# Kernel tuning notes

Hardware: AMD Instinct MI355X
Metric: run time of the kernel (lower is better)

Reference implementation:

```python
import jax, jax.numpy as jnp
import numpy as np

D_MODEL = 1024
PATCH = 16
HID = 256
VOCAB = 256

def setup_inputs() -> dict:
    key = jax.random.key(0)
    ks = jax.random.split(key, 12)
    B, N = 16, 512
    s = lambda *sh: 1.0 / np.sqrt(sh[-1])
    inp = {
        'latents': jax.random.normal(ks[0], (B, N, D_MODEL), dtype=jnp.float32),
        'target_bytes': jax.random.randint(ks[1], (B, N * PATCH), 0, VOCAB, dtype=jnp.int64),
        'W_proj': jax.random.normal(ks[2], (HID, D_MODEL), dtype=jnp.float32) * s(HID, D_MODEL),
        'b_proj': jnp.zeros((HID,), dtype=jnp.float32),
        'emb_table': jax.random.normal(ks[3], (VOCAB, HID), dtype=jnp.float32),
        'W_ih': jax.random.normal(ks[4], (3 * HID, 2 * HID), dtype=jnp.float32) * s(1, 2 * HID),
        'W_hh': jax.random.normal(ks[5], (3 * HID, HID), dtype=jnp.float32) * s(1, HID),
        'b_ih': jnp.zeros((3 * HID,), dtype=jnp.float32),
        'b_hh': jnp.zeros((3 * HID,), dtype=jnp.float32),
        'W_head': jax.random.normal(ks[6], (VOCAB, HID), dtype=jnp.float32) * s(VOCAB, HID),
        'b_head': jnp.zeros((VOCAB,), dtype=jnp.float32),
    }
    return inp

def _gru_scan(x_proj, W_hh, b_hh, h0):
    # x_proj: [T, BN, 3H] precomputed input projections (incl. b_ih)
    def step(h, xg):
        hg = h @ W_hh.T + b_hh                      # [BN, 3H]
        xr, xz, xn = jnp.split(xg, 3, axis=-1)
        hr, hz, hn = jnp.split(hg, 3, axis=-1)
        r = jax.nn.sigmoid(xr + hr)
        z = jax.nn.sigmoid(xz + hz)
        n = jnp.tanh(xn + r * hn)
        h_new = (1.0 - z) * n + z * h
        return h_new, h_new
    _, outs = jax.lax.scan(step, h0, x_proj)
    return outs                                      # [T, BN, H]

def reference(latents, target_bytes, W_proj, b_proj, emb_table, W_ih, W_hh, b_ih, b_hh, W_head, b_head):
    B, N, D = latents.shape
    BN = B * N
    latent_ctx = (latents.reshape(BN, D) @ W_proj.T + b_proj)        # [BN, H]
    targets = target_bytes.reshape(BN, PATCH)
    sos = jnp.zeros((BN, 1), dtype=targets.dtype)
    rnn_in_bytes = jnp.concatenate([sos, targets[:, :-1]], axis=1)   # [BN, P]
    emb = emb_table[rnn_in_bytes]                                    # [BN, P, H]
    lat_exp = jnp.broadcast_to(latent_ctx[:, None, :], (BN, PATCH, HID))
    rnn_input = jnp.concatenate([emb, lat_exp], axis=-1)             # [BN, P, 2H]
    x_proj = jnp.einsum('bpi,gi->bpg', rnn_input, W_ih) + b_ih       # [BN, P, 3H]
    h0 = jnp.zeros((BN, HID), dtype=latents.dtype)
    outs = _gru_scan(jnp.swapaxes(x_proj, 0, 1), W_hh, b_hh, h0)     # [P, BN, H]
    outs = jnp.swapaxes(outs, 0, 1)                                  # [BN, P, H]
    logits = jnp.einsum('bph,vh->bpv', outs, W_head) + b_head        # [BN, P, 256]
    return logits.reshape(B, N, PATCH, VOCAB)
```

## Files before the change

### kernel.cpp

```cpp
#include <hip/hip_runtime.h>
#include <math.h>

#define NSEQ 8192
#define PATCHL 16
#define HIDN 256
#define VOCABN 256

typedef __attribute__((ext_vector_type(4))) float f32x4;
typedef __attribute__((ext_vector_type(8))) short bf16x8;

__device__ __forceinline__ unsigned short f2bf(float f) {
    unsigned int x = __float_as_uint(f);
    unsigned int r = (x + 0x7fffu + ((x >> 16) & 1u)) >> 16;
    return (unsigned short)r;
}
__device__ __forceinline__ float bf2f(unsigned short b) {
    return __uint_as_float(((unsigned int)b) << 16);
}
__device__ __forceinline__ float sigf(float x)   { return 1.f / (1.f + __expf(-x)); }
__device__ __forceinline__ float tanhf_(float x) { return 2.f / (1.f + __expf(-2.f * x)) - 1.f; }

__global__ __launch_bounds__(256)
void pack_frag(const float* __restrict__ src, int ld, int col0, int nks,
               unsigned short* __restrict__ dst)
{
    const int g = blockIdx.x * 256 + threadIdx.x;
    const int lane = g & 63;
    const int ks = (g / 64) % nks;
    const int T  = g / (64 * nks);
    const float* s = src + (size_t)(T * 16 + (lane & 15)) * ld + col0 + ks * 32 + ((lane >> 4) & 3) * 8;
    unsigned int q[4];
#pragma unroll
    for (int j = 0; j < 4; j++) {
        unsigned int lo = f2bf(s[2 * j]);
        unsigned int hi = f2bf(s[2 * j + 1]);
        q[j] = lo | (hi << 16);
    }
    uint4 v; v.x = q[0]; v.y = q[1]; v.z = q[2]; v.w = q[3];
    *(uint4*)(dst + (size_t)g * 8) = v;
}

template<bool ASRC_BF16, bool OUT_BF16>
__global__ __launch_bounds__(512)
void gemm_mfma(const void* __restrict__ Asrc, int lda,
               const unsigned short* __restrict__ bpack, int nks_total,
               const float* __restrict__ bias, void* __restrict__ Cdst, int ldc,
               int K)
{
    const int tid = threadIdx.x;
    const int w = tid >> 6, lane = tid & 63;
    const int l15 = lane & 15, kg = (lane >> 4) & 3;
    const int bm = blockIdx.x * 128, bn = blockIdx.y * 64;

    __shared__ unsigned short As[2][128 * 64];

    const int srow = tid >> 2;
    const int scol = (tid & 3) * 16;
    const int nkt = K / 64;

    f32x4 acc[4];
#pragma unroll
    for (int nt = 0; nt < 4; nt++) acc[nt] = 0.f;

    const int wb0 = srow * 128 + ((scol * 2) ^ ((srow & 7) << 4));
    const int wb1 = srow * 128 + ((scol * 2 + 16) ^ ((srow & 7) << 4));

#define STAGE(kt, buf) do {                                                         \
        const int gk = (kt) * 64 + scol;                                            \
        unsigned short tmp[16];                                                     \
        if (ASRC_BF16) {                                                            \
            const unsigned short* A = (const unsigned short*)Asrc;                  \
            *(uint4*)(tmp)     = *(const uint4*)(A + (size_t)(bm + srow) * lda + gk);      \
            *(uint4*)(tmp + 8) = *(const uint4*)(A + (size_t)(bm + srow) * lda + gk + 8);  \
        } else {                                                                    \
            const float* A = (const float*)Asrc;                                    \
            const float4 a0 = *(const float4*)(A + (size_t)(bm + srow) * lda + gk);       \
            const float4 a1 = *(const float4*)(A + (size_t)(bm + srow) * lda + gk + 4);   \
            const float4 a2 = *(const float4*)(A + (size_t)(bm + srow) * lda + gk + 8);   \
            const float4 a3 = *(const float4*)(A + (size_t)(bm + srow) * lda + gk + 12);  \
            tmp[0] = f2bf(a0.x);  tmp[1] = f2bf(a0.y);  tmp[2] = f2bf(a0.z);  tmp[3] = f2bf(a0.w);   \
            tmp[4] = f2bf(a1.x);  tmp[5] = f2bf(a1.y);  tmp[6] = f2bf(a1.z);  tmp[7] = f2bf(a1.w);   \
            tmp[8] = f2bf(a2.x);  tmp[9] = f2bf(a2.y);  tmp[10] = f2bf(a2.z); tmp[11] = f2bf(a2.w);  \
            tmp[12] = f2bf(a3.x); tmp[13] = f2bf(a3.y); tmp[14] = f2bf(a3.z); tmp[15] = f2bf(a3.w);  \
        }                                                                           \
        *(uint4*)((char*)As[buf] + wb0) = *(uint4*)tmp;                             \
        *(uint4*)((char*)As[buf] + wb1) = *(uint4*)(tmp + 8);                       \
    } while (0)

    STAGE(0, 0);
    __syncthreads();

    for (int kt = 0; kt < nkt; ++kt) {
        if (kt + 1 < nkt) STAGE(kt + 1, (kt + 1) & 1);
        const unsigned short* buf = As[kt & 1];
        const int row = w * 16 + l15;
#pragma unroll
        for (int ks = 0; ks < 2; ++ks) {
            const int bo = row * 128 + (((ks * 64) + kg * 16) ^ ((row & 7) << 4));
            const bf16x8 a = *(const bf16x8*)((const char*)buf + bo);
#pragma unroll
            for (int nt = 0; nt < 4; ++nt) {
                const int T = blockIdx.y * 4 + nt;
                const bf16x8 b = *(const bf16x8*)(bpack + (((size_t)T * nks_total + (kt * 2 + ks)) * 64 + lane) * 8);
                acc[nt] = __builtin_amdgcn_mfma_f32_16x16x32_bf16(a, b, acc[nt], 0, 0, 0);
            }
        }
        __syncthreads();
    }
#undef STAGE

#pragma unroll
    for (int nt = 0; nt < 4; ++nt) {
        const int n = bn + nt * 16 + l15;
        const float bv = bias ? bias[n] : 0.f;
#pragma unroll
        for (int rr = 0; rr < 4; ++rr) {
            const int m = bm + w * 16 + kg * 4 + rr;
            const float v = acc[nt][rr] + bv;
            if (OUT_BF16) ((unsigned short*)Cdst)[(size_t)m * ldc + n] = f2bf(v);
            else          ((float*)Cdst)[(size_t)m * ldc + n] = v;
        }
    }
}

__global__ __launch_bounds__(512)
void xg_producer(const int* __restrict__ bytes,
                 const float* __restrict__ latg,
                 const unsigned short* __restrict__ premixB,
                 unsigned short* __restrict__ xg,
                 int seq0)
{
    __shared__ unsigned short PM[256 * 256];
    __shared__ int BY[32 * 16];

    const int tid = threadIdx.x;
    const int g = blockIdx.y;
    const int sblk = seq0 + blockIdx.x * 32;

#pragma unroll
    for (int j = 0; j < 16; ++j) {
        const int idx = j * 512 + tid;
        const int flat = idx * 8;
        const int bv = flat >> 8, u = flat & 255;
        *(uint4*)(PM + flat) = *(const uint4*)(premixB + (size_t)bv * 768 + g * 256 + u);
    }
    BY[tid & 511] = bytes[(size_t)sblk * PATCHL + (tid & 511)];
    __syncthreads();

    const int ug = (tid & 63) * 4;
    const int sg = tid >> 6;

    for (int si = 0; si < 4; ++si) {
        const int sl = si * 8 + sg;
        const int seq = sblk + sl;
        const float4 lat = *(const float4*)(latg + (size_t)seq * 768 + g * 256 + ug);
        unsigned short* dst = xg + ((size_t)(seq - seq0) * PATCHL) * 768 + g * 256 + ug;
#pragma unroll
        for (int p = 0; p < PATCHL; ++p) {
            const int bv = p ? BY[sl * PATCHL + p - 1] : 0;
            const ushort4 pm = *(const ushort4*)(PM + bv * 256 + ug);
            ushort4 o;
            o.x = f2bf(lat.x + bf2f(pm.x));
            o.y = f2bf(lat.y + bf2f(pm.y));
            o.z = f2bf(lat.z + bf2f(pm.z));
            o.w = f2bf(lat.w + bf2f(pm.w));
            *(ushort4*)(dst + (size_t)p * 768) = o;
        }
    }
}

#define XGS 776
__global__ __launch_bounds__(512, 4)
void gru_scan(const unsigned short* __restrict__ xg,
              const unsigned short* __restrict__ wpack,
              const float* __restrict__ b_hh,
              unsigned short* __restrict__ hh)
{
    const int tid  = threadIdx.x;
    const int w    = tid >> 6;
    const int lane = tid & 63;
    const int l15  = lane & 15;
    const int kg   = (lane >> 4) & 3;
    const int s0l  = blockIdx.x * 32;

    __shared__ unsigned short XG[32 * XGS];
    __shared__ unsigned short H0[32 * 256];
    __shared__ unsigned short H1[32 * 256];

    float bhr[2], bhz[2], bhn[2];
#pragma unroll
    for (int nt = 0; nt < 2; nt++) {
        const int u = w * 32 + nt * 16 + l15;
        bhr[nt] = b_hh[u]; bhz[nt] = b_hh[256 + u]; bhn[nt] = b_hh[512 + u];
    }

    float hreg[2][2][4];
#pragma unroll
    for (int mt = 0; mt < 2; mt++)
#pragma unroll
        for (int nt = 0; nt < 2; nt++)
#pragma unroll
            for (int rr = 0; rr < 4; rr++) hreg[mt][nt][rr] = 0.f;

    unsigned short* Hcur = H0;
    unsigned short* Hnxt = H1;

    for (int p = 0; p < PATCHL; ++p) {
#pragma unroll
        for (int j = 0; j < 6; ++j) {
            const int idx = j * 512 + tid;
            const int row = idx / 96, col = idx % 96;
            *(uint4*)(XG + row * XGS + col * 8) =
                *(const uint4*)(xg + ((size_t)(s0l + row) * PATCHL + p) * 768 + col * 8);
        }
        __syncthreads();

        f32x4 accr[2][2], accz[2][2], accn[2][2];
#pragma unroll
        for (int mt = 0; mt < 2; mt++)
#pragma unroll
            for (int nt = 0; nt < 2; nt++) {
                accr[mt][nt] = 0.f; accz[mt][nt] = 0.f; accn[mt][nt] = 0.f;
            }
        if (p != 0) {
#pragma unroll
            for (int ks = 0; ks < 8; ++ks) {
                bf16x8 a[2];
#pragma unroll
                for (int mt = 0; mt < 2; mt++) {
                    const int s = mt * 16 + l15;
                    const int off = (ks * 64 + kg * 16) ^ ((s & 7) << 4);
                    a[mt] = *(const bf16x8*)(Hcur + s * 256 + (off >> 1));
                }
#pragma unroll
                for (int nt = 0; nt < 2; nt++) {
                    const int tb = w * 2 + nt;
                    const bf16x8 br = *(const bf16x8*)(wpack + (((size_t)(tb)      * 8 + ks) * 64 + lane) * 8);
                    const bf16x8 bz = *(const bf16x8*)(wpack + (((size_t)(16 + tb) * 8 + ks) * 64 + lane) * 8);
                    const bf16x8 bn = *(const bf16x8*)(wpack + (((size_t)(32 + tb) * 8 + ks) * 64 + lane) * 8);
#pragma unroll
                    for (int mt = 0; mt < 2; mt++) {
                        accr[mt][nt] = __builtin_amdgcn_mfma_f32_16x16x32_bf16(a[mt], br, accr[mt][nt], 0, 0, 0);
                        accz[mt][nt] = __builtin_amdgcn_mfma_f32_16x16x32_bf16(a[mt], bz, accz[mt][nt], 0, 0, 0);
                        accn[mt][nt] = __builtin_amdgcn_mfma_f32_16x16x32_bf16(a[mt], bn, accn[mt][nt], 0, 0, 0);
                    }
                }
            }
        }
#pragma unroll
        for (int mt = 0; mt < 2; mt++)
#pragma unroll
            for (int nt = 0; nt < 2; nt++) {
                const int u = w * 32 + nt * 16 + l15;
#pragma unroll
                for (int rr = 0; rr < 4; rr++) {
                    const int sl = mt * 16 + kg * 4 + rr;
                    const float xr = bf2f(XG[sl * XGS + u]);
                    const float xz = bf2f(XG[sl * XGS + 256 + u]);
                    const float xn = bf2f(XG[sl * XGS + 512 + u]);
                    const float r = sigf(xr + accr[mt][nt][rr] + bhr[nt]);
                    const float z = sigf(xz + accz[mt][nt][rr] + bhz[nt]);
                    const float n = tanhf_(xn + r * (accn[mt][nt][rr] + bhn[nt]));
                    const float hn_ = (1.f - z) * n + z * hreg[mt][nt][rr];
                    hreg[mt][nt][rr] = hn_;
                    const int bo = (2 * u) ^ ((sl & 7) << 4);
                    Hnxt[sl * 256 + (bo >> 1)] = f2bf(hn_);
                }
            }
        __syncthreads();

#pragma unroll
        for (int rj = 0; rj < 4; ++rj) {
            const int row = w * 4 + rj;
            const int boff = (lane * 8) ^ ((row & 7) << 4);
            const ushort4 v = *(const ushort4*)((const char*)(Hnxt + row * 256) + boff);
            *(ushort4*)(hh + ((size_t)(s0l + row) * PATCHL + p) * 256 + lane * 4) = v;
        }

        unsigned short* t_ = Hcur; Hcur = Hnxt; Hnxt = t_;
    }
}

extern "C" void kernel_launch(void* const* d_in, const int* in_sizes, int n_in,
                              void* d_out, int out_size, void* d_ws, size_t ws_size,
                              hipStream_t stream)
{
    const float* latents = (const float*)d_in[0];
    const int*   tb      = (const int*)d_in[1];
    const float* W_proj  = (const float*)d_in[2];
    const float* b_proj  = (const float*)d_in[3];
    const float* emb     = (const float*)d_in[4];
    const float* W_ih    = (const float*)d_in[5];
    const float* W_hh    = (const float*)d_in[6];
    const float* b_ih    = (const float*)d_in[7];
    const float* b_hh    = (const float*)d_in[8];
    const float* W_head  = (const float*)d_in[9];
    const float* b_head  = (const float*)d_in[10];
    float* out = (float*)d_out;

    char* w = (char*)d_ws;
    float* latg = (float*)w;                               w += (size_t)NSEQ * 768 * 4;
    unsigned short* ctxb    = (unsigned short*)w;          w += (size_t)NSEQ * HIDN * 2;
    unsigned short* premixB = (unsigned short*)w;          w += 256 * 768 * 2;
    unsigned short* bpack1  = (unsigned short*)w;          w += 16 * 32 * 64 * 8 * 2;
    unsigned short* bpack2  = (unsigned short*)w;          w += 48 * 8 * 64 * 8 * 2;
    unsigned short* bpack3  = (unsigned short*)w;          w += 48 * 8 * 64 * 8 * 2;
    unsigned short* wpackG  = (unsigned short*)w;          w += 48 * 8 * 64 * 8 * 2;
    unsigned short* bpackH  = (unsigned short*)w;          w += 16 * 8 * 64 * 8 * 2;
    unsigned short* xg_c    = (unsigned short*)w;
    const size_t fixed_bytes = (size_t)(w - (char*)d_ws);
    const size_t chunk_full  = (size_t)NSEQ * PATCHL * (768 + 256) * 2;

    int nch = 1;
    while (nch < 16 && fixed_bytes + chunk_full / nch > ws_size) nch <<= 1;
    const int SPC = NSEQ / nch;
    unsigned short* hh_c = xg_c + (size_t)SPC * PATCHL * 768;

    hipLaunchKernelGGL(pack_frag, dim3(128), dim3(256), 0, stream, W_proj, 1024, 0, 32, bpack1);
    hipLaunchKernelGGL(pack_frag, dim3(96),  dim3(256), 0, stream, W_ih,   512, 256, 8, bpack2);
    hipLaunchKernelGGL(pack_frag, dim3(96),  dim3(256), 0, stream, W_ih,   512, 0,   8, bpack3);
    hipLaunchKernelGGL(pack_frag, dim3(96),  dim3(256), 0, stream, W_hh,   256, 0,   8, wpackG);
    hipLaunchKernelGGL(pack_frag, dim3(32),  dim3(256), 0, stream, W_head, 256, 0,   8, bpackH);

    hipLaunchKernelGGL((gemm_mfma<false, true>), dim3(2, 12), dim3(512), 0, stream,
                       emb, 256, bpack3, 8, nullptr, premixB, 768, 256);
    hipLaunchKernelGGL((gemm_mfma<false, true>), dim3(NSEQ / 128, 4), dim3(512), 0, stream,
                       latents, 1024, bpack1, 32, b_proj, ctxb, 256, 1024);
    hipLaunchKernelGGL((gemm_mfma<true, false>), dim3(NSEQ / 128, 12), dim3(512), 0, stream,
                       ctxb, 256, bpack2, 8, b_ih, latg, 768, 256);

    for (int c = 0; c < nch; ++c) {
        const int seq0 = c * SPC;
        hipLaunchKernelGGL(xg_producer, dim3(SPC / 32, 3), dim3(512), 0, stream,
                           tb, latg, premixB, xg_c, seq0);
        hipLaunchKernelGGL(gru_scan, dim3(SPC / 32), dim3(512), 0, stream,
                           xg_c, wpackG, b_hh, hh_c);
        hipLaunchKernelGGL((gemm_mfma<true, false>), dim3(SPC * PATCHL / 128, 4), dim3(512), 0, stream,
                           hh_c, 256, bpackH, 8, b_head,
                           out + (size_t)seq0 * PATCHL * VOCABN, 256, 256);
    }
}
```

Measured before the change: 410.6 us.

## Fuse input-gate producer into GRU scan and single-buffer hidden state

Removes the separate xg_producer kernel and its large bf16 intermediate buffer. The GRU scan now gathers per-byte premix rows from premixB into shared memory each step and adds latent gate contributions held in registers, with b_hh folded in for the r and z gates. The double-buffered H tile becomes a single buffer, with an extra barrier and the hh writeback deferred by one step. This cuts global write and read traffic of the xg tensor and shrinks the workspace so fewer chunks are needed. In exchange it adds register pressure from the latent arrays and does the premix gathers inside the serial scan.

```diff
diff --git a/kernel.cpp b/kernel.cpp
--- a/kernel.cpp
+++ b/kernel.cpp
@@ -123,58 +123,15 @@
     }
 }
 
-__global__ __launch_bounds__(512)
-void xg_producer(const int* __restrict__ bytes,
-                 const float* __restrict__ latg,
-                 const unsigned short* __restrict__ premixB,
-                 unsigned short* __restrict__ xg,
-                 int seq0)
-{
-    __shared__ unsigned short PM[256 * 256];
-    __shared__ int BY[32 * 16];
-
-    const int tid = threadIdx.x;
-    const int g = blockIdx.y;
-    const int sblk = seq0 + blockIdx.x * 32;
-
-#pragma unroll
-    for (int j = 0; j < 16; ++j) {
-        const int idx = j * 512 + tid;
-        const int flat = idx * 8;
-        const int bv = flat >> 8, u = flat & 255;
-        *(uint4*)(PM + flat) = *(const uint4*)(premixB + (size_t)bv * 768 + g * 256 + u);
-    }
-    BY[tid & 511] = bytes[(size_t)sblk * PATCHL + (tid & 511)];
-    __syncthreads();
-
-    const int ug = (tid & 63) * 4;
-    const int sg = tid >> 6;
-
-    for (int si = 0; si < 4; ++si) {
-        const int sl = si * 8 + sg;
-        const int seq = sblk + sl;
-        const float4 lat = *(const float4*)(latg + (size_t)seq * 768 + g * 256 + ug);
-        unsigned short* dst = xg + ((size_t)(seq - seq0) * PATCHL) * 768 + g * 256 + ug;
-#pragma unroll
-        for (int p = 0; p < PATCHL; ++p) {
-            const int bv = p ? BY[sl * PATCHL + p - 1] : 0;
-            const ushort4 pm = *(const ushort4*)(PM + bv * 256 + ug);
-            ushort4 o;
-            o.x = f2bf(lat.x + bf2f(pm.x));
-            o.y = f2bf(lat.y + bf2f(pm.y));
-            o.z = f2bf(lat.z + bf2f(pm.z));
-            o.w = f2bf(lat.w + bf2f(pm.w));
-            *(ushort4*)(dst + (size_t)p * 768) = o;
-        }
-    }
-}
-
-#define XGS 776
+#define PMS 776
 __global__ __launch_bounds__(512, 4)
-void gru_scan(const unsigned short* __restrict__ xg,
-              const unsigned short* __restrict__ wpack,
-              const float* __restrict__ b_hh,
-              unsigned short* __restrict__ hh)
+void gru_scan_fused(const int* __restrict__ bytes,
+                    const float* __restrict__ latg,
+                    const unsigned short* __restrict__ premixB,
+                    const unsigned short* __restrict__ wpack,
+                    const float* __restrict__ b_hh,
+                    unsigned short* __restrict__ hh,
+                    int seq0)
 {
     const int tid  = threadIdx.x;
     const int w    = tid >> 6;
@@ -182,10 +139,13 @@
     const int l15  = lane & 15;
     const int kg   = (lane >> 4) & 3;
     const int s0l  = blockIdx.x * 32;
-
-    __shared__ unsigned short XG[32 * XGS];
-    __shared__ unsigned short H0[32 * 256];
-    __shared__ unsigned short H1[32 * 256];
+    const int s0g  = seq0 + s0l;
+
+    __shared__ unsigned short PMs[32 * PMS];
+    __shared__ unsigned short H[32 * 256];
+    __shared__ int BYs[512];
+
+    BYs[tid] = bytes[(size_t)s0g * PATCHL + tid];
 
     float bhr[2], bhz[2], bhn[2];
 #pragma unroll
@@ -194,6 +154,22 @@
         bhr[nt] = b_hh[u]; bhz[nt] = b_hh[256 + u]; bhn[nt] = b_hh[512 + u];
     }
 
+    float lgr[2][2][4], lgz[2][2][4], lgn[2][2][4];
+#pragma unroll
+    for (int mt = 0; mt < 2; mt++)
+#pragma unroll
+        for (int nt = 0; nt < 2; nt++) {
+            const int u = w * 32 + nt * 16 + l15;
+#pragma unroll
+            for (int rr = 0; rr < 4; rr++) {
+                const int sg = s0g + mt * 16 + kg * 4 + rr;
+                const float* lg = latg + (size_t)sg * 768;
+                lgr[mt][nt][rr] = lg[u]       + bhr[nt];
+                lgz[mt][nt][rr] = lg[u + 256] + bhz[nt];
+                lgn[mt][nt][rr] = lg[u + 512];
+            }
+        }
+
     float hreg[2][2][4];
 #pragma unroll
     for (int mt = 0; mt < 2; mt++)
@@ -202,18 +178,27 @@
 #pragma unroll
             for (int rr = 0; rr < 4; rr++) hreg[mt][nt][rr] = 0.f;
 
-    unsigned short* Hcur = H0;
-    unsigned short* Hnxt = H1;
+    __syncthreads();
 
     for (int p = 0; p < PATCHL; ++p) {
 #pragma unroll
         for (int j = 0; j < 6; ++j) {
             const int idx = j * 512 + tid;
-            const int row = idx / 96, col = idx % 96;
-            *(uint4*)(XG + row * XGS + col * 8) =
-                *(const uint4*)(xg + ((size_t)(s0l + row) * PATCHL + p) * 768 + col * 8);
-        }
-        __syncthreads();
+            const int row = idx / 96, col = idx - row * 96;
+            const int bv = p ? BYs[row * PATCHL + p - 1] : 0;
+            *(uint4*)(PMs + row * PMS + col * 8) =
+                *(const uint4*)(premixB + (size_t)bv * 768 + col * 8);
+        }
+
+        if (p) {
+#pragma unroll
+            for (int rj = 0; rj < 4; ++rj) {
+                const int row = w * 4 + rj;
+                const int boff = (lane * 8) ^ ((row & 7) << 4);
+                const ushort4 v = *(const ushort4*)((const char*)(H + row * 256) + boff);
+                *(ushort4*)(hh + ((size_t)(s0l + row) * PATCHL + (p - 1)) * 256 + lane * 4) = v;
+            }
+        }
 
         f32x4 accr[2][2], accz[2][2], accn[2][2];
 #pragma unroll
@@ -230,7 +215,7 @@
                 for (int mt = 0; mt < 2; mt++) {
                     const int s = mt * 16 + l15;
                     const int off = (ks * 64 + kg * 16) ^ ((s & 7) << 4);
-                    a[mt] = *(const bf16x8*)(Hcur + s * 256 + (off >> 1));
+                    a[mt] = *(const bf16x8*)(H + s * 256 + (off >> 1));
                 }
 #pragma unroll
                 for (int nt = 0; nt < 2; nt++) {
@@ -247,6 +232,8 @@
                 }
             }
         }
+        __syncthreads();
+
 #pragma unroll
         for (int mt = 0; mt < 2; mt++)
 #pragma unroll
@@ -255,29 +242,27 @@
 #pragma unroll
                 for (int rr = 0; rr < 4; rr++) {
                     const int sl = mt * 16 + kg * 4 + rr;
-                    const float xr = bf2f(XG[sl * XGS + u]);
-                    const float xz = bf2f(XG[sl * XGS + 256 + u]);
-                    const float xn = bf2f(XG[sl * XGS + 512 + u]);
-                    const float r = sigf(xr + accr[mt][nt][rr] + bhr[nt]);
-                    const float z = sigf(xz + accz[mt][nt][rr] + bhz[nt]);
+                    const float xr = lgr[mt][nt][rr] + bf2f(PMs[sl * PMS + u]);
+                    const float xz = lgz[mt][nt][rr] + bf2f(PMs[sl * PMS + 256 + u]);
+                    const float xn = lgn[mt][nt][rr] + bf2f(PMs[sl * PMS + 512 + u]);
+                    const float r = sigf(xr + accr[mt][nt][rr]);
+                    const float z = sigf(xz + accz[mt][nt][rr]);
                     const float n = tanhf_(xn + r * (accn[mt][nt][rr] + bhn[nt]));
                     const float hn_ = (1.f - z) * n + z * hreg[mt][nt][rr];
                     hreg[mt][nt][rr] = hn_;
                     const int bo = (2 * u) ^ ((sl & 7) << 4);
-                    Hnxt[sl * 256 + (bo >> 1)] = f2bf(hn_);
+                    H[sl * 256 + (bo >> 1)] = f2bf(hn_);
                 }
             }
         __syncthreads();
-
-#pragma unroll
-        for (int rj = 0; rj < 4; ++rj) {
-            const int row = w * 4 + rj;
-            const int boff = (lane * 8) ^ ((row & 7) << 4);
-            const ushort4 v = *(const ushort4*)((const char*)(Hnxt + row * 256) + boff);
-            *(ushort4*)(hh + ((size_t)(s0l + row) * PATCHL + p) * 256 + lane * 4) = v;
-        }
-
-        unsigned short* t_ = Hcur; Hcur = Hnxt; Hnxt = t_;
+    }
+
+#pragma unroll
+    for (int rj = 0; rj < 4; ++rj) {
+        const int row = w * 4 + rj;
+        const int boff = (lane * 8) ^ ((row & 7) << 4);
+        const ushort4 v = *(const ushort4*)((const char*)(H + row * 256) + boff);
+        *(ushort4*)(hh + ((size_t)(s0l + row) * PATCHL + (PATCHL - 1)) * 256 + lane * 4) = v;
     }
 }
 
@@ -307,14 +292,13 @@
     unsigned short* bpack3  = (unsigned short*)w;          w += 48 * 8 * 64 * 8 * 2;
     unsigned short* wpackG  = (unsigned short*)w;          w += 48 * 8 * 64 * 8 * 2;
     unsigned short* bpackH  = (unsigned short*)w;          w += 16 * 8 * 64 * 8 * 2;
-    unsigned short* xg_c    = (unsigned short*)w;
+    unsigned short* hh_c    = (unsigned short*)w;
     const size_t fixed_bytes = (size_t)(w - (char*)d_ws);
-    const size_t chunk_full  = (size_t)NSEQ * PATCHL * (768 + 256) * 2;
+    const size_t chunk_full  = (size_t)NSEQ * PATCHL * 256 * 2;
 
     int nch = 1;
     while (nch < 16 && fixed_bytes + chunk_full / nch > ws_size) nch <<= 1;
     const int SPC = NSEQ / nch;
-    unsigned short* hh_c = xg_c + (size_t)SPC * PATCHL * 768;
 
     hipLaunchKernelGGL(pack_frag, dim3(128), dim3(256), 0, stream, W_proj, 1024, 0, 32, bpack1);
     hipLaunchKernelGGL(pack_frag, dim3(96),  dim3(256), 0, stream, W_ih,   512, 256, 8, bpack2);
@@ -331,10 +315,8 @@
 
     for (int c = 0; c < nch; ++c) {
         const int seq0 = c * SPC;
-        hipLaunchKernelGGL(xg_producer, dim3(SPC / 32, 3), dim3(512), 0, stream,
-                           tb, latg, premixB, xg_c, seq0);
-        hipLaunchKernelGGL(gru_scan, dim3(SPC / 32), dim3(512), 0, stream,
-                           xg_c, wpackG, b_hh, hh_c);
+        hipLaunchKernelGGL(gru_scan_fused, dim3(SPC / 32), dim3(512), 0, stream,
+                           tb, latg, premixB, wpackG, b_hh, hh_c, seq0);
         hipLaunchKernelGGL((gemm_mfma<true, false>), dim3(SPC * PATCHL / 128, 4), dim3(512), 0, stream,
                            hh_c, 256, bpackH, 8, b_head,
                            out + (size_t)seq0 * PATCHL * VOCABN, 256, 256);
```

Result: slower. 679.5 us (+65.5%).
